# Optimization experiments

Measured on AMD Instinct MI355X. Metric: run time of the kernel, lower is better.

Reference implementation:

```python
import jax, jax.numpy as jnp
import numpy as np

B, N, D, H = 4, 2048, 1024, 16
HD = D // H


def setup_inputs() -> dict:
    key = jax.random.key(0)
    ks = jax.random.split(key, 9)
    s = 1.0 / np.sqrt(D)
    return {
        "x": jax.random.normal(ks[0], (B, N, D), jnp.float32),
        "Wq": jax.random.normal(ks[1], (D, D), jnp.float32) * s,
        "bq": jnp.zeros((D,), jnp.float32),
        "Wk": jax.random.normal(ks[2], (D, D), jnp.float32) * s,
        "bk": jnp.zeros((D,), jnp.float32),
        "Wv": jax.random.normal(ks[3], (D, D), jnp.float32) * s,
        "bv": jnp.zeros((D,), jnp.float32),
        "Wo": jax.random.normal(ks[4], (D, D), jnp.float32) * s,
        "bo": jnp.zeros((D,), jnp.float32),
    }


def reference(x, Wq, bq, Wk, bk, Wv, bv, Wo, bo):
    Bx, Nx, Dx = x.shape
    q = x @ Wq + bq  # [B,N,D]
    k = x @ Wk + bk
    v = x @ Wv + bv
    # split heads -> [B,H,N,hd]
    q = q.reshape(Bx, Nx, H, HD).transpose(0, 2, 1, 3)
    k = k.reshape(Bx, Nx, H, HD).transpose(0, 2, 1, 3)
    v = v.reshape(Bx, Nx, H, HD).transpose(0, 2, 1, 3)
    q = q / jnp.sqrt(jnp.asarray(HD, q.dtype))
    scores = jnp.einsum("bhqd,bhkd->bhqk", q, k)
    # causal mask: additive -1e9 strictly above diagonal (matches torch.triu diag=1)
    mask = jnp.triu(jnp.full((Nx, Nx), -1e9, dtype=scores.dtype), k=1)
    probs = jax.nn.softmax(scores + mask, axis=-1)
    out = jnp.einsum("bhqk,bhkd->bhqd", probs, v)  # [B,H,N,hd]
    out = out.transpose(0, 2, 1, 3).reshape(Bx, Nx, Dx)  # concat heads
    return out @ Wo + bo
```

## Files before the change

### kernel.cpp

```cpp
#include <hip/hip_runtime.h>
#include <hip/hip_bf16.h>


#define BB 4
#define NN 2048
#define DD 1024
#define HH 16
#define HD 64
#define MM (BB * NN)

typedef __bf16 bf16;
typedef __bf16 bf16x4 __attribute__((ext_vector_type(4)));
typedef __bf16 bf16x8 __attribute__((ext_vector_type(8)));
typedef float f32x4 __attribute__((ext_vector_type(4)));

__device__ __forceinline__ void async_copy16(bf16* lds, const bf16* g) {
    __builtin_amdgcn_global_load_lds(
        (const __attribute__((address_space(1))) void*)g,
        (__attribute__((address_space(3))) void*)lds, 16, 0, 0);
}

__global__ void prep(const float* __restrict__ x,
                     const float* __restrict__ W0, const float* __restrict__ W1,
                     const float* __restrict__ W2, const float* __restrict__ W3,
                     bf16* __restrict__ xb, bf16* __restrict__ Wt) {
    __shared__ float tile[32][33];
    if (blockIdx.z == 0) {
        int i = (blockIdx.x * 256 + threadIdx.x) * 8;
        float4 a = *(const float4*)&x[i];
        float4 b = *(const float4*)&x[i + 4];
        bf16x8 o;
        o[0] = (bf16)a.x; o[1] = (bf16)a.y; o[2] = (bf16)a.z; o[3] = (bf16)a.w;
        o[4] = (bf16)b.x; o[5] = (bf16)b.y; o[6] = (bf16)b.z; o[7] = (bf16)b.w;
        *(bf16x8*)&xb[i] = o;
    } else {
        int wz = blockIdx.x >> 10;
        int by = (blockIdx.x >> 5) & 31;
        int bx = blockIdx.x & 31;
        const float* W = (wz == 0) ? W0 : (wz == 1) ? W1 : (wz == 2) ? W2 : W3;
        bf16* out = Wt + (size_t)wz * DD * DD;
        int tx = threadIdx.x & 31, ty = threadIdx.x >> 5;
        int x0 = bx * 32, y0 = by * 32;
#pragma unroll
        for (int i = 0; i < 32; i += 8)
            tile[ty + i][tx] = W[(size_t)(y0 + ty + i) * DD + x0 + tx];
        __syncthreads();
#pragma unroll
        for (int i = 0; i < 32; i += 8)
            out[(size_t)(x0 + ty + i) * DD + y0 + tx] = (bf16)tile[tx][ty + i];
    }
}

template <int MODE>
__global__ __launch_bounds__(256) void gemm_bt(
    const bf16* __restrict__ A, const bf16* __restrict__ Wt,
    const float* __restrict__ b0, const float* __restrict__ b1,
    const float* __restrict__ b2, void* __restrict__ out0,
    void* __restrict__ out1, void* __restrict__ out2) {
    const int K = DD;
    __shared__ __align__(16) bf16 smem[MODE == 0 ? 128 * 136 : 128 * 64];
    bf16* As = smem;
    bf16* Bs = smem + 128 * 32;
    bf16* Cs = smem;

    int m0 = blockIdx.x * 128;
    int n0 = blockIdx.y * 128;

    const bf16* Wz;
    const float* bias;
    void* out;
    float scale = 1.0f;
    int z = 0;
    if (MODE == 0) {
        z = blockIdx.z;
        Wz = Wt + (size_t)z * DD * DD;
        bias = (z == 0) ? b0 : ((z == 1) ? b1 : b2);
        out = (z == 0) ? out0 : ((z == 1) ? out1 : out2);
        if (z == 0) scale = 0.125f * 1.44269504f;
    } else {
        Wz = Wt; bias = b0; out = out0;
    }

    int tid = threadIdx.x;
    int w = tid >> 6, lane = tid & 63;
    int wm = w >> 1, wn = w & 1;
    int quad = lane >> 4, l16 = lane & 15;

    f32x4 acc[4][4];
#pragma unroll
    for (int i = 0; i < 4; i++)
#pragma unroll
        for (int j = 0; j < 4; j++) acc[i][j] = (f32x4){0.f, 0.f, 0.f, 0.f};

    for (int k0 = 0; k0 < K; k0 += 32) {
        __syncthreads();
#pragma unroll
        for (int j = 0; j < 2; j++) {
            int c = j * 256 + w * 64 + lane;
            int row = c >> 2, kk = (c & 3) * 8;
            async_copy16(&As[c * 8], &A[(size_t)(m0 + row) * K + k0 + kk]);
            async_copy16(&Bs[c * 8], &Wz[(size_t)(n0 + row) * K + k0 + kk]);
        }
        __syncthreads();

        bf16x8 af[4], bfm[4];
#pragma unroll
        for (int i = 0; i < 4; i++) {
            af[i] = *(const bf16x8*)&As[(wm * 64 + i * 16 + l16) * 32 + quad * 8];
            bfm[i] = *(const bf16x8*)&Bs[(wn * 64 + i * 16 + l16) * 32 + quad * 8];
        }
#pragma unroll
        for (int i = 0; i < 4; i++)
#pragma unroll
            for (int j = 0; j < 4; j++)
                acc[i][j] = __builtin_amdgcn_mfma_f32_16x16x32_bf16(
                    af[i], bfm[j], acc[i][j], 0, 0, 0);
    }

    if (MODE == 0) {
        __syncthreads();
#pragma unroll
        for (int j = 0; j < 4; j++) {
            int nl = wn * 64 + j * 16 + l16;
            float bv = bias[n0 + nl];
#pragma unroll
            for (int i = 0; i < 4; i++) {
#pragma unroll
                for (int r = 0; r < 4; r++) {
                    int ml = wm * 64 + i * 16 + quad * 4 + r;
                    bf16 v = (bf16)((acc[i][j][r] + bv) * scale);
                    if (z == 2) Cs[nl * 136 + ml] = v;
                    else        Cs[ml * 136 + nl] = v;
                }
            }
        }
        __syncthreads();

        int bidx = m0 >> 11;
        int tok0 = m0 & (NN - 1);
        int hh0 = n0 >> 6;
        if (z != 2) {
#pragma unroll
            for (int hf = 0; hf < 2; hf++) {
                bf16* base = (bf16*)out + ((size_t)(bidx * HH + hh0 + hf) * NN + tok0) * HD;
#pragma unroll
                for (int k = 0; k < 4; k++) {
                    int f = k * 2048 + tid * 8;
                    int tok = f >> 6, hd = f & 63;
                    *(bf16x8*)&base[f] = *(const bf16x8*)&Cs[tok * 136 + hf * 64 + hd];
                }
            }
        } else {
#pragma unroll
            for (int hf = 0; hf < 2; hf++) {
#pragma unroll
                for (int k = 0; k < 4; k++) {
                    int hd = k * 16 + (tid >> 4);
                    int p0 = (tid & 15) * 8;
                    int base32 = p0 & ~31;
                    int qq = (p0 & 31) >> 3;
                    const bf16* crow = &Cs[(hf * 64 + hd) * 136];
                    bf16x4 lo = *(const bf16x4*)&crow[base32 + qq * 4];
                    bf16x4 hi = *(const bf16x4*)&crow[base32 + qq * 4 + 16];
                    bf16x8 v = __builtin_shufflevector(lo, hi, 0, 1, 2, 3, 4, 5, 6, 7);
                    bf16* dst = (bf16*)out +
                        ((size_t)(bidx * HH + hh0 + hf) * HD + hd) * NN + tok0 + p0;
                    *(bf16x8*)dst = v;
                }
            }
        }
    } else {
#pragma unroll
        for (int j = 0; j < 4; j++) {
            int n = n0 + wn * 64 + j * 16 + l16;
            float bv = bias[n];
#pragma unroll
            for (int i = 0; i < 4; i++) {
                int mrow = m0 + wm * 64 + i * 16 + quad * 4;
#pragma unroll
                for (int r = 0; r < 4; r++)
                    ((float*)out)[(size_t)(mrow + r) * DD + n] = acc[i][j][r] + bv;
            }
        }
    }
}

__global__ __launch_bounds__(256, 4) void flash_attn(
    const bf16* __restrict__ Q, const bf16* __restrict__ Kg,
    const bf16* __restrict__ Vt_g, bf16* __restrict__ Oc) {
    __shared__ __align__(16) bf16 Ks[2][64 * 72];
    __shared__ __align__(16) bf16 Vs[2][64 * 72];

    int bh = blockIdx.x;
    int b = bh >> 4, h = bh & 15;
    int tid = threadIdx.x;
    int w = tid >> 6, lane = tid & 63;
    int quad = lane >> 4, l16 = lane & 15;

    const bf16* Qb = Q + (size_t)bh * NN * HD;
    const bf16* Kb = Kg + (size_t)bh * NN * HD;
    const bf16* Vtb = Vt_g + (size_t)bh * HD * NN;

    bf16x8 ones8;
#pragma unroll
    for (int i = 0; i < 8; i++) ones8[i] = (bf16)1.0f;

    int kr[2], kc[2];
#pragma unroll
    for (int j = 0; j < 2; j++) {
        int c = j * 256 + tid;
        kr[j] = c >> 3; kc[j] = (c & 7) * 8;
    }

    for (int phase = 0; phase < 2; phase++) {
        int qj = (phase == 0) ? blockIdx.y : (31 - blockIdx.y);
        int q0 = qj * 64;
        int qrow = q0 + w * 16 + l16;

        bf16x8 qf[2];
#pragma unroll
        for (int ks = 0; ks < 2; ks++)
            qf[ks] = *(const bf16x8*)&Qb[(size_t)qrow * HD + ks * 32 + quad * 8];

        f32x4 l_sum = (f32x4){0.f, 0.f, 0.f, 0.f};
        f32x4 o_acc[4];
#pragma unroll
        for (int di = 0; di < 4; di++) o_acc[di] = (f32x4){0.f, 0.f, 0.f, 0.f};

        bf16x8 kreg[2], vreg[2];
#pragma unroll
        for (int j = 0; j < 2; j++) {
            kreg[j] = *(const bf16x8*)&Kb[(size_t)kr[j] * HD + kc[j]];
            vreg[j] = *(const bf16x8*)&Vtb[(size_t)kr[j] * NN + kc[j]];
        }
#pragma unroll
        for (int j = 0; j < 2; j++) {
            *(bf16x8*)&Ks[0][kr[j] * 72 + kc[j]] = kreg[j];
            *(bf16x8*)&Vs[0][kr[j] * 72 + kc[j]] = vreg[j];
        }
        __syncthreads();

        for (int t = 0; t <= qj; t++) {
            int cur = t & 1;
            if (t < qj) {
                int kvn = (t + 1) * 64;
#pragma unroll
                for (int j = 0; j < 2; j++) {
                    kreg[j] = *(const bf16x8*)&Kb[(size_t)(kvn + kr[j]) * HD + kc[j]];
                    vreg[j] = *(const bf16x8*)&Vtb[(size_t)kr[j] * NN + kvn + kc[j]];
                }
            }

            const bf16* Kcur = Ks[cur];
            const bf16* Vcur = Vs[cur];
            int kv0 = t * 64;
            bool diag = (t == qj);
#pragma unroll
            for (int mi = 0; mi < 2; mi++) {
                int ba = 2 * mi, bb = 2 * mi + 1;
                bf16x8 ka0 = *(const bf16x8*)&Kcur[(ba * 16 + l16) * 72 + quad * 8];
                bf16x8 ka1 = *(const bf16x8*)&Kcur[(ba * 16 + l16) * 72 + 32 + quad * 8];
                bf16x8 kb0 = *(const bf16x8*)&Kcur[(bb * 16 + l16) * 72 + quad * 8];
                bf16x8 kb1 = *(const bf16x8*)&Kcur[(bb * 16 + l16) * 72 + 32 + quad * 8];
                f32x4 sa = (f32x4){0.f, 0.f, 0.f, 0.f};
                f32x4 sb = (f32x4){0.f, 0.f, 0.f, 0.f};
                sa = __builtin_amdgcn_mfma_f32_16x16x32_bf16(ka0, qf[0], sa, 0, 0, 0);
                sa = __builtin_amdgcn_mfma_f32_16x16x32_bf16(ka1, qf[1], sa, 0, 0, 0);
                sb = __builtin_amdgcn_mfma_f32_16x16x32_bf16(kb0, qf[0], sb, 0, 0, 0);
                sb = __builtin_amdgcn_mfma_f32_16x16x32_bf16(kb1, qf[1], sb, 0, 0, 0);
                bf16x4 pa4, pb4;
                if (diag) {
                    int kva = kv0 + ba * 16 + quad * 4;
                    int kvb = kv0 + bb * 16 + quad * 4;
#pragma unroll
                    for (int r = 0; r < 4; r++) {
                        pa4[r] = (bf16)((kva + r > qrow) ? 0.f : exp2f(sa[r]));
                        pb4[r] = (bf16)((kvb + r > qrow) ? 0.f : exp2f(sb[r]));
                    }
                } else {
#pragma unroll
                    for (int r = 0; r < 4; r++) {
                        pa4[r] = (bf16)exp2f(sa[r]);
                        pb4[r] = (bf16)exp2f(sb[r]);
                    }
                }
                bf16x8 pfrag = __builtin_shufflevector(pa4, pb4, 0, 1, 2, 3, 4, 5, 6, 7);
                l_sum = __builtin_amdgcn_mfma_f32_16x16x32_bf16(pfrag, ones8, l_sum, 0, 0, 0);
#pragma unroll
                for (int di = 0; di < 4; di++) {
                    bf16x8 vfrag = *(const bf16x8*)&Vcur[(di * 16 + l16) * 72 + mi * 32 + quad * 8];
                    o_acc[di] = __builtin_amdgcn_mfma_f32_16x16x32_bf16(pfrag, vfrag, o_acc[di], 0, 0, 0);
                }
            }

            if (t < qj) {
                bf16* Kn = Ks[cur ^ 1];
                bf16* Vn = Vs[cur ^ 1];
#pragma unroll
                for (int j = 0; j < 2; j++) {
                    *(bf16x8*)&Kn[kr[j] * 72 + kc[j]] = kreg[j];
                    *(bf16x8*)&Vn[kr[j] * 72 + kc[j]] = vreg[j];
                }
            }
            __syncthreads();
        }

#pragma unroll
        for (int r = 0; r < 4; r++) {
            float inv = 1.0f / l_sum[r];
            int tok = q0 + w * 16 + quad * 4 + r;
#pragma unroll
            for (int di = 0; di < 4; di++) {
                int d = h * 64 + di * 16 + l16;
                Oc[((size_t)(b * NN + tok)) * DD + d] = (bf16)(o_acc[di][r] * inv);
            }
        }
    }
}

extern "C" void kernel_launch(void* const* d_in, const int* in_sizes, int n_in,
                              void* d_out, int out_size, void* d_ws, size_t ws_size,
                              hipStream_t stream) {
    const float* x  = (const float*)d_in[0];
    const float* Wq = (const float*)d_in[1];
    const float* bq = (const float*)d_in[2];
    const float* Wk = (const float*)d_in[3];
    const float* bk = (const float*)d_in[4];
    const float* Wv = (const float*)d_in[5];
    const float* bv = (const float*)d_in[6];
    const float* Wo = (const float*)d_in[7];
    const float* bo = (const float*)d_in[8];

    const size_t need = (size_t)(8388608ull * 5 + 4194304ull) * sizeof(bf16);
    if (ws_size < need) return;

    bf16* ws = (bf16*)d_ws;
    bf16* xb = ws;
    bf16* wt = xb + (size_t)MM * DD;
    bf16* Qw = wt + 4ull * DD * DD;
    bf16* Kw = Qw + (size_t)MM * DD;
    bf16* Vw = Kw + (size_t)MM * DD;
    bf16* Aw = Vw + (size_t)MM * DD;

    prep<<<dim3(4096, 1, 2), 256, 0, stream>>>(x, Wq, Wk, Wv, Wo, xb, wt);

    gemm_bt<0><<<dim3(MM / 128, DD / 128, 3), 256, 0, stream>>>(
        xb, wt, bq, bk, bv, Qw, Kw, Vw);

    flash_attn<<<dim3(BB * HH, 16), 256, 0, stream>>>(Qw, Kw, Vw, Aw);

    gemm_bt<1><<<dim3(MM / 128, DD / 128, 1), 256, 0, stream>>>(
        Aw, wt + 3ull * DD * DD, bo, bo, bo, d_out, d_out, d_out);
}
```

Before: 252.2 us.

## Enlarge QKV GEMM tile to 256x128 with 512-thread blocks

```diff
diff --git a/kernel.cpp b/kernel.cpp
--- a/kernel.cpp
+++ b/kernel.cpp
@@ -51,35 +51,24 @@
     }
 }
 
-template <int MODE>
-__global__ __launch_bounds__(256) void gemm_bt(
+__global__ __launch_bounds__(512, 6) void gemm_qkv(
     const bf16* __restrict__ A, const bf16* __restrict__ Wt,
     const float* __restrict__ b0, const float* __restrict__ b1,
-    const float* __restrict__ b2, void* __restrict__ out0,
-    void* __restrict__ out1, void* __restrict__ out2) {
+    const float* __restrict__ b2, bf16* __restrict__ out0,
+    bf16* __restrict__ out1, bf16* __restrict__ out2) {
     const int K = DD;
-    __shared__ __align__(16) bf16 smem[MODE == 0 ? 128 * 136 : 128 * 64];
+    __shared__ __align__(16) bf16 smem[128 * 136];
     bf16* As = smem;
-    bf16* Bs = smem + 128 * 32;
+    bf16* Bs = smem + 256 * 32;
     bf16* Cs = smem;
 
-    int m0 = blockIdx.x * 128;
+    int m0 = blockIdx.x * 256;
     int n0 = blockIdx.y * 128;
-
-    const bf16* Wz;
-    const float* bias;
-    void* out;
-    float scale = 1.0f;
-    int z = 0;
-    if (MODE == 0) {
-        z = blockIdx.z;
-        Wz = Wt + (size_t)z * DD * DD;
-        bias = (z == 0) ? b0 : ((z == 1) ? b1 : b2);
-        out = (z == 0) ? out0 : ((z == 1) ? out1 : out2);
-        if (z == 0) scale = 0.125f * 1.44269504f;
-    } else {
-        Wz = Wt; bias = b0; out = out0;
-    }
+    int z = blockIdx.z;
+    const bf16* Wz = Wt + (size_t)z * DD * DD;
+    const float* bias = (z == 0) ? b0 : ((z == 1) ? b1 : b2);
+    bf16* out = (z == 0) ? out0 : ((z == 1) ? out1 : out2);
+    float scale = (z == 0) ? 0.125f * 1.44269504f : 1.0f;
 
     int tid = threadIdx.x;
     int w = tid >> 6, lane = tid & 63;
@@ -96,10 +85,121 @@
         __syncthreads();
 #pragma unroll
         for (int j = 0; j < 2; j++) {
+            int c = j * 512 + tid;
+            int row = c >> 2, kk = (c & 3) * 8;
+            async_copy16(&As[c * 8], &A[(size_t)(m0 + row) * K + k0 + kk]);
+        }
+        {
+            int row = tid >> 2, kk = (tid & 3) * 8;
+            async_copy16(&Bs[tid * 8], &Wz[(size_t)(n0 + row) * K + k0 + kk]);
+        }
+        __syncthreads();
+
+        bf16x8 af[4], bfm[4];
+#pragma unroll
+        for (int i = 0; i < 4; i++) {
+            af[i] = *(const bf16x8*)&As[(wm * 64 + i * 16 + l16) * 32 + quad * 8];
+            bfm[i] = *(const bf16x8*)&Bs[(wn * 64 + i * 16 + l16) * 32 + quad * 8];
+        }
+#pragma unroll
+        for (int i = 0; i < 4; i++)
+#pragma unroll
+            for (int j = 0; j < 4; j++)
+                acc[i][j] = __builtin_amdgcn_mfma_f32_16x16x32_bf16(
+                    af[i], bfm[j], acc[i][j], 0, 0, 0);
+    }
+
+    int bidx = m0 >> 11;
+    int tok0 = m0 & (NN - 1);
+    int hh0 = n0 >> 6;
+    __syncthreads();
+
+#pragma unroll
+    for (int pp = 0; pp < 2; pp++) {
+        if (pp) __syncthreads();
+        if ((wm >> 1) == pp) {
+#pragma unroll
+            for (int j = 0; j < 4; j++) {
+                int nl = wn * 64 + j * 16 + l16;
+                float bv = bias[n0 + nl];
+#pragma unroll
+                for (int i = 0; i < 4; i++) {
+#pragma unroll
+                    for (int r = 0; r < 4; r++) {
+                        int mloc = (wm & 1) * 64 + i * 16 + quad * 4 + r;
+                        bf16 v = (bf16)((acc[i][j][r] + bv) * scale);
+                        if (z == 2) Cs[nl * 136 + mloc] = v;
+                        else        Cs[mloc * 136 + nl] = v;
+                    }
+                }
+            }
+        }
+        __syncthreads();
+
+        if (z != 2) {
+#pragma unroll
+            for (int hf = 0; hf < 2; hf++) {
+                bf16* base = out +
+                    ((size_t)(bidx * HH + hh0 + hf) * NN + tok0 + pp * 128) * HD;
+#pragma unroll
+                for (int k = 0; k < 2; k++) {
+                    int f = k * 4096 + tid * 8;
+                    *(bf16x8*)&base[f] =
+                        *(const bf16x8*)&Cs[(f >> 6) * 136 + hf * 64 + (f & 63)];
+                }
+            }
+        } else {
+#pragma unroll
+            for (int k = 0; k < 4; k++) {
+                int idx = k * 4096 + tid * 8;
+                int nl = idx >> 7;
+                int p0 = idx & 127;
+                int hf = nl >> 6, hd = nl & 63;
+                int base32 = p0 & ~31;
+                int qq = (p0 & 31) >> 3;
+                const bf16* crow = &Cs[nl * 136];
+                bf16x4 lo = *(const bf16x4*)&crow[base32 + qq * 4];
+                bf16x4 hi = *(const bf16x4*)&crow[base32 + qq * 4 + 16];
+                bf16x8 v = __builtin_shufflevector(lo, hi, 0, 1, 2, 3, 4, 5, 6, 7);
+                bf16* dst = out +
+                    ((size_t)(bidx * HH + hh0 + hf) * HD + hd) * NN +
+                    tok0 + pp * 128 + p0;
+                *(bf16x8*)dst = v;
+            }
+        }
+    }
+}
+
+__global__ __launch_bounds__(256) void gemm_out(
+    const bf16* __restrict__ A, const bf16* __restrict__ Wt,
+    const float* __restrict__ bias, float* __restrict__ out) {
+    const int K = DD;
+    __shared__ __align__(16) bf16 smem[128 * 64];
+    bf16* As = smem;
+    bf16* Bs = smem + 128 * 32;
+
+    int m0 = blockIdx.x * 128;
+    int n0 = blockIdx.y * 128;
+
+    int tid = threadIdx.x;
+    int w = tid >> 6, lane = tid & 63;
+    int wm = w >> 1, wn = w & 1;
+    int quad = lane >> 4, l16 = lane & 15;
+
+    f32x4 acc[4][4];
+#pragma unroll
+    for (int i = 0; i < 4; i++)
+#pragma unroll
+        for (int j = 0; j < 4; j++) acc[i][j] = (f32x4){0.f, 0.f, 0.f, 0.f};
+
+    for (int k0 = 0; k0 < K; k0 += 32) {
+        __syncthreads();
+#pragma unroll
+        for (int j = 0; j < 2; j++) {
             int c = j * 256 + w * 64 + lane;
             int row = c >> 2, kk = (c & 3) * 8;
             async_copy16(&As[c * 8], &A[(size_t)(m0 + row) * K + k0 + kk]);
-            async_copy16(&Bs[c * 8], &Wz[(size_t)(n0 + row) * K + k0 + kk]);
+            async_copy16(&Bs[c * 8], &Wt[(size_t)(n0 + row) * K + k0 + kk]);
         }
         __syncthreads();
 
@@ -117,70 +217,16 @@
                     af[i], bfm[j], acc[i][j], 0, 0, 0);
     }
 
-    if (MODE == 0) {
-        __syncthreads();
-#pragma unroll
-        for (int j = 0; j < 4; j++) {
-            int nl = wn * 64 + j * 16 + l16;
-            float bv = bias[n0 + nl];
-#pragma unroll
-            for (int i = 0; i < 4; i++) {
-#pragma unroll
-                for (int r = 0; r < 4; r++) {
-                    int ml = wm * 64 + i * 16 + quad * 4 + r;
-                    bf16 v = (bf16)((acc[i][j][r] + bv) * scale);
-                    if (z == 2) Cs[nl * 136 + ml] = v;
-                    else        Cs[ml * 136 + nl] = v;
-                }
-            }
-        }
-        __syncthreads();
-
-        int bidx = m0 >> 11;
-        int tok0 = m0 & (NN - 1);
-        int hh0 = n0 >> 6;
-        if (z != 2) {
-#pragma unroll
-            for (int hf = 0; hf < 2; hf++) {
-                bf16* base = (bf16*)out + ((size_t)(bidx * HH + hh0 + hf) * NN + tok0) * HD;
-#pragma unroll
-                for (int k = 0; k < 4; k++) {
-                    int f = k * 2048 + tid * 8;
-                    int tok = f >> 6, hd = f & 63;
-                    *(bf16x8*)&base[f] = *(const bf16x8*)&Cs[tok * 136 + hf * 64 + hd];
-                }
-            }
-        } else {
-#pragma unroll
-            for (int hf = 0; hf < 2; hf++) {
-#pragma unroll
-                for (int k = 0; k < 4; k++) {
-                    int hd = k * 16 + (tid >> 4);
-                    int p0 = (tid & 15) * 8;
-                    int base32 = p0 & ~31;
-                    int qq = (p0 & 31) >> 3;
-                    const bf16* crow = &Cs[(hf * 64 + hd) * 136];
-                    bf16x4 lo = *(const bf16x4*)&crow[base32 + qq * 4];
-                    bf16x4 hi = *(const bf16x4*)&crow[base32 + qq * 4 + 16];
-                    bf16x8 v = __builtin_shufflevector(lo, hi, 0, 1, 2, 3, 4, 5, 6, 7);
-                    bf16* dst = (bf16*)out +
-                        ((size_t)(bidx * HH + hh0 + hf) * HD + hd) * NN + tok0 + p0;
-                    *(bf16x8*)dst = v;
-                }
-            }
-        }
-    } else {
-#pragma unroll
-        for (int j = 0; j < 4; j++) {
-            int n = n0 + wn * 64 + j * 16 + l16;
-            float bv = bias[n];
-#pragma unroll
-            for (int i = 0; i < 4; i++) {
-                int mrow = m0 + wm * 64 + i * 16 + quad * 4;
-#pragma unroll
-                for (int r = 0; r < 4; r++)
-                    ((float*)out)[(size_t)(mrow + r) * DD + n] = acc[i][j][r] + bv;
-            }
+#pragma unroll
+    for (int j = 0; j < 4; j++) {
+        int n = n0 + wn * 64 + j * 16 + l16;
+        float bv = bias[n];
+#pragma unroll
+        for (int i = 0; i < 4; i++) {
+            int mrow = m0 + wm * 64 + i * 16 + quad * 4;
+#pragma unroll
+            for (int r = 0; r < 4; r++)
+                out[(size_t)(mrow + r) * DD + n] = acc[i][j][r] + bv;
         }
     }
 }
@@ -344,11 +390,11 @@
 
     prep<<<dim3(4096, 1, 2), 256, 0, stream>>>(x, Wq, Wk, Wv, Wo, xb, wt);
 
-    gemm_bt<0><<<dim3(MM / 128, DD / 128, 3), 256, 0, stream>>>(
+    gemm_qkv<<<dim3(MM / 256, DD / 128, 3), 512, 0, stream>>>(
         xb, wt, bq, bk, bv, Qw, Kw, Vw);
 
     flash_attn<<<dim3(BB * HH, 16), 256, 0, stream>>>(Qw, Kw, Vw, Aw);
 
-    gemm_bt<1><<<dim3(MM / 128, DD / 128, 1), 256, 0, stream>>>(
-        Aw, wt + 3ull * DD * DD, bo, bo, bo, d_out, d_out, d_out);
-}
+    gemm_out<<<dim3(MM / 128, DD / 128), 256, 0, stream>>>(
+        Aw, wt + 3ull * DD * DD, bo, (float*)d_out);
+}
```

New measurement: 607.7 us. 2.41x slower.
